# Kernel tuning notes

Hardware: AMD Instinct MI355X
Metric: run time of the kernel (lower is better)

## Reference

```python
import jax, jax.numpy as jnp
import numpy as np

B, T_PAST, T_FUT, GH, GW = 256, 20, 30, 100, 100
HID = 32  # past_encoder_dim


def gru_cell(x, h, w_ih, w_hh, b_ih, b_hh):
    # torch nn.GRU single-cell math; weights [3H, in], [3H, H]
    gi = x @ w_ih.T + b_ih
    gh = h @ w_hh.T + b_hh
    i_r, i_z, i_n = jnp.split(gi, 3, axis=-1)
    h_r, h_z, h_n = jnp.split(gh, 3, axis=-1)
    r = jax.nn.sigmoid(i_r + h_r)
    zg = jax.nn.sigmoid(i_z + h_z)
    n = jnp.tanh(i_n + r * h_n)
    return (1.0 - zg) * n + zg * h


def bilinear(grid, q):
    # grid [B,H,W,C]; q [B,2], dim 0 -> height, dim 1 -> width (matches torch code)
    Bn, Hh, Ww, C = grid.shape
    fy = jnp.clip(jnp.floor(q[:, 0]), 0.0, Hh - 2).astype(jnp.int32)
    fx = jnp.clip(jnp.floor(q[:, 1]), 0.0, Ww - 2).astype(jnp.int32)
    ay = jnp.clip(q[:, 0] - fy, 0.0, 1.0)[:, None]
    ax = jnp.clip(q[:, 1] - fx, 0.0, 1.0)[:, None]
    b = jnp.arange(Bn)
    tl = grid[b, fy, fx]
    tr = grid[b, fy, fx + 1]
    bl = grid[b, fy + 1, fx]
    br = grid[b, fy + 1, fx + 1]
    top = tl + ax * (tr - tl)
    bot = bl + ax * (br - bl)
    return top + ay * (bot - top)  # [B,C]


def setup_inputs() -> dict:
    key = jax.random.key(0)
    ks = jax.random.split(key, 24)
    s = 0.05
    f32 = jnp.float32
    inp = {
        'z': jax.random.normal(ks[0], (B, T_FUT, 2), f32),
        'player_past': jax.random.uniform(ks[1], (B, T_PAST, 2), f32) * (GH - 10),
        'lidar': jax.random.normal(ks[2], (B, GH, GW, 2), f32),
        'conv0_w': jax.random.normal(ks[3], (2, 2, 2, 32), f32) * s,   # HWIO
        'conv0_b': jnp.zeros((32,), f32),
        'conv1_w': jax.random.normal(ks[4], (2, 2, 32, 32), f32) * s,
        'conv1_b': jnp.zeros((32,), f32),
        'conv2_w': jax.random.normal(ks[5], (2, 2, 32, 32), f32) * s,
        'conv2_b': jnp.zeros((32,), f32),
        'conv3_w': jax.random.normal(ks[6], (2, 2, 32, 32), f32) * s,
        'conv3_b': jnp.zeros((32,), f32),
        'enc_wih': jax.random.normal(ks[7], (3 * HID, 2), f32) * s,
        'enc_whh': jax.random.normal(ks[8], (3 * HID, HID), f32) * s,
        'enc_bih': jnp.zeros((3 * HID,), f32),
        'enc_bhh': jnp.zeros((3 * HID,), f32),
        'dec_wih': jax.random.normal(ks[9], (3 * HID, HID + 2), f32) * s,
        'dec_whh': jax.random.normal(ks[10], (3 * HID, HID), f32) * s,
        'dec_bih': jnp.zeros((3 * HID,), f32),
        'dec_bhh': jnp.zeros((3 * HID,), f32),
        'mlp_w1': jax.random.normal(ks[11], (512, HID), f32) * s,
        'mlp_b1': jnp.zeros((512,), f32),
        'mlp_w2': jax.random.normal(ks[12], (4, 512), f32) * s,
        'mlp_b2': jnp.zeros((4,), f32),
    }
    return inp


def reference(z, player_past, lidar,
              conv0_w, conv0_b, conv1_w, conv1_b, conv2_w, conv2_b, conv3_w, conv3_b,
              enc_wih, enc_whh, enc_bih, enc_bhh,
              dec_wih, dec_whh, dec_bih, dec_bhh,
              mlp_w1, mlp_b1, mlp_w2, mlp_b2):
    # field model: ZeroPad2d((0,1,0,1)) + Conv 2x2 + ReLU, x4 -> same-size NHWC conv
    v = lidar
    for w, b in ((conv0_w, conv0_b), (conv1_w, conv1_b), (conv2_w, conv2_b), (conv3_w, conv3_b)):
        v = jax.nn.relu(jax.lax.conv_general_dilated(
            v, w, (1, 1), [(0, 1), (0, 1)],
            dimension_numbers=('NHWC', 'HWIO', 'NHWC')) + b)
    context_lidar = v  # [B,GH,GW,32]

    # past encoder GRU; last output of single-layer GRU == final hidden
    h0 = jnp.zeros((z.shape[0], HID), z.dtype)
    def enc_step(h, x_t):
        return gru_cell(x_t, h, enc_wih, enc_whh, enc_bih, enc_bhh), None
    h_enc, _ = jax.lax.scan(enc_step, h0, jnp.swapaxes(player_past, 0, 1))

    y_tm2 = player_past[:, -2, :]
    y_tm1 = player_past[:, -1, :]

    def dec_step(carry, z_t):
        h, y1, y2 = carry
        interp_t = bilinear(context_lidar, y1)                 # [B,32]
        x = jnp.concatenate([y1, interp_t], axis=-1)            # [B,34]
        h = gru_cell(x, h, dec_wih, dec_whh, dec_bih, dec_bhh)
        # locscale_mlp: Linear(32,512) -> Linear(512,4) (no ReLU between, per source)
        ls = (h @ mlp_w1.T + mlp_b1) @ mlp_w2.T + mlp_b2
        loc = ls[:, :2]
        scale = jax.nn.softplus(ls[:, 2:])
        y_t = 2.0 * y1 - y2 + loc + scale * z_t                 # verlet + affine sample
        return (h, y_t, y1), (y_t, scale)

    _, (ys, scales) = jax.lax.scan(dec_step, (h_enc, y_tm1, y_tm2), jnp.swapaxes(z, 0, 1))
    y = jnp.swapaxes(ys, 0, 1)          # [B,T,2]
    scales = jnp.swapaxes(scales, 0, 1)  # [B,T,2]
    logabsdet = jnp.sum(jnp.log(jnp.abs(jnp.prod(scales, axis=-2))), axis=-1)  # [B]
    return (y, logabsdet)
```

## Files before the change

### kernel.cpp

```cpp
#include <hip/hip_runtime.h>
#include <math.h>

typedef __attribute__((ext_vector_type(8))) short    short8;
typedef __attribute__((ext_vector_type(4))) float    f32x4;
typedef __attribute__((ext_vector_type(4))) unsigned uint4v;

#define FRAG0 256

__device__ __forceinline__ unsigned short f2bf(float f) {
    unsigned u = __builtin_bit_cast(unsigned, f);
    u = u + 0x7fffu + ((u >> 16) & 1u);
    return (unsigned short)(u >> 16);
}
__device__ __forceinline__ unsigned packRNE(float hi, float lo) {
    return (unsigned)f2bf(lo) | ((unsigned)f2bf(hi) << 16);
}
__device__ __forceinline__ unsigned pack_trunc(float hi, float lo) {
    return __builtin_amdgcn_perm(__builtin_bit_cast(unsigned, hi),
                                 __builtin_bit_cast(unsigned, lo), 0x07060302u);
}
__device__ __forceinline__ float rfl(float x) {
    return __builtin_bit_cast(float, __builtin_amdgcn_readfirstlane(__builtin_bit_cast(int, x)));
}
__device__ __forceinline__ f32x4 mfma16(short8 a, short8 b, f32x4 c) {
    return __builtin_amdgcn_mfma_f32_16x16x32_bf16(a, b, c, 0, 0, 0);
}
__device__ __forceinline__ unsigned bperm(int addr, unsigned v) {
    return (unsigned)__builtin_amdgcn_ds_bpermute(addr, (int)v);
}
template<int PAT>
__device__ __forceinline__ float swzXf(float v) {
    return __builtin_bit_cast(float, __builtin_amdgcn_ds_swizzle(__builtin_bit_cast(int, v), PAT));
}
__device__ __forceinline__ unsigned swz1u(unsigned v){ return (unsigned)__builtin_amdgcn_ds_swizzle((int)v, 0x041F); }
__device__ __forceinline__ float sigf(float x) { return __builtin_amdgcn_rcpf(1.f + __expf(-x)); }
__device__ __forceinline__ float tanhfast(float x) {
    float e = __expf(2.f * x);
    return 1.f - 2.f * __builtin_amdgcn_rcpf(e + 1.f);
}
__device__ __forceinline__ f32x4 ld4(const float* p) { return *(const f32x4*)p; }

__device__ __forceinline__ void packC(unsigned* P, f32x4 a0, f32x4 a1, bool oob) {
    float r0 = fmaxf(a0[0], 0.f), r1 = fmaxf(a0[1], 0.f), r2 = fmaxf(a0[2], 0.f), r3 = fmaxf(a0[3], 0.f);
    float s0 = fmaxf(a1[0], 0.f), s1 = fmaxf(a1[1], 0.f), s2 = fmaxf(a1[2], 0.f), s3 = fmaxf(a1[3], 0.f);
    P[0] = pack_trunc(r1, r0); P[1] = pack_trunc(r3, r2);
    P[2] = pack_trunc(s1, s0); P[3] = pack_trunc(s3, s2);
    if (oob) { P[0] = 0u; P[1] = 0u; P[2] = 0u; P[3] = 0u; }
}

__global__ __launch_bounds__(256) void r2p2_prep(
    const float* __restrict__ w0, const float* __restrict__ w1,
    const float* __restrict__ w2, const float* __restrict__ w3,
    const float* __restrict__ enc_whh,
    const float* __restrict__ dec_wih, const float* __restrict__ dec_whh,
    const float* __restrict__ mw1, const float* __restrict__ mb1,
    const float* __restrict__ mw2, const float* __restrict__ mb2,
    float* __restrict__ wsf, unsigned* __restrict__ wsu) {
    const int tid = threadIdx.x, bx = blockIdx.x;
    if (bx == 0) {
        __shared__ float red[64];
        if (tid < 128) {
            int k = tid & 31, j = tid >> 5;
            const float* w2r = mw2 + j * 512;
            float a0 = 0.f, a1 = 0.f, a2 = 0.f, a3 = 0.f;
#pragma unroll 4
            for (int m = 0; m < 512; m += 4) {
                a0 = fmaf(w2r[m],     mw1[m * 32 + k],       a0);
                a1 = fmaf(w2r[m + 1], mw1[(m + 1) * 32 + k], a1);
                a2 = fmaf(w2r[m + 2], mw1[(m + 2) * 32 + k], a2);
                a3 = fmaf(w2r[m + 3], mw1[(m + 3) * 32 + k], a3);
            }
            wsf[j * 32 + k] = (a0 + a1) + (a2 + a3);
        } else if (tid < 192) {
            int t = tid - 128;
            int j = t & 3, ch = t >> 2;
            const float* w2c = mw2 + j * 512 + ch * 32;
            const float* b1c = mb1 + ch * 32;
            float p = 0.f;
#pragma unroll 8
            for (int m = 0; m < 32; ++m) p = fmaf(w2c[m], b1c[m], p);
            red[t] = p;
        }
        __syncthreads();
        if (tid < 4) {
            float c = mb2[tid];
#pragma unroll
            for (int i = 0; i < 16; ++i) c += red[tid + i * 4];
            wsf[128 + tid] = c;
        }
        return;
    }
    int base = (bx - 1) * 416;
    for (int c = base + tid; c < base + 416 && c < 2816; c += 256) {
        int f = c >> 6, lane = c & 63;
        int n = lane & 15, q = lane >> 4;
        int pc0 = ((n >> 2) << 3) | (n & 3);
        float v[8];
        if (f < 2) {
            int co = pc0 + f * 4;
#pragma unroll
            for (int j = 0; j < 8; ++j) v[j] = (q == 0) ? w0[j * 32 + co] : 0.f;
        } else if (f < 26) {
            int t = f - 2;
            const float* W = (t < 8) ? w1 : (t < 16) ? w2 : w3;
            t &= 7;
            int mt = t >> 2, ks = t & 3, co = pc0 + mt * 4;
#pragma unroll
            for (int j = 0; j < 8; ++j) v[j] = W[(ks * 32 + q * 8 + j) * 32 + co];
        } else if (f < 32) {
            int t = f - 26, gate = t >> 1, mt = t & 1;
            int row = gate * 32 + pc0 + mt * 4;
#pragma unroll
            for (int j = 0; j < 8; ++j) v[j] = dec_wih[row * 34 + 2 + q * 8 + j];
        } else if (f < 38) {
            int t = f - 32, gate = t >> 1, mt = t & 1;
            int row = gate * 32 + pc0 + mt * 4;
#pragma unroll
            for (int j = 0; j < 8; ++j) v[j] = dec_whh[row * 32 + q * 8 + j];
        } else {
            int t = f - 38, gate = t >> 1, mt = t & 1;
            int row = gate * 32 + pc0 + mt * 4;
#pragma unroll
            for (int j = 0; j < 8; ++j) v[j] = enc_whh[row * 32 + q * 8 + j];
        }
        uint4v u;
        u[0] = packRNE(v[1], v[0]); u[1] = packRNE(v[3], v[2]);
        u[2] = packRNE(v[5], v[4]); u[3] = packRNE(v[7], v[6]);
        *(uint4v*)(wsu + FRAG0 + f * 256 + lane * 4) = u;
    }
}

__global__ __launch_bounds__(256)
void r2p2_main(
    const float* __restrict__ z, const float* __restrict__ past, const float* __restrict__ lidar,
    const float* __restrict__ b0, const float* __restrict__ b1,
    const float* __restrict__ b2, const float* __restrict__ b3,
    const float* __restrict__ enc_wih, const float* __restrict__ enc_bih, const float* __restrict__ enc_bhh,
    const float* __restrict__ dec_wih, const float* __restrict__ dec_bih, const float* __restrict__ dec_bhh,
    const float* __restrict__ wsf, const unsigned* __restrict__ wsu,
    float* __restrict__ out) {

    const int tid = threadIdx.x, b = blockIdx.x;
    const int wid = tid >> 6, lane = tid & 63;
    const int n = lane & 15, q = lane >> 4, e = n & 1;

    __shared__ __align__(16) unsigned sLID[104 * 104];
    __shared__ __align__(16) float PASTs[40];
    __shared__ __align__(16) float ZVs[64];

    if (wid != 0) {
        int st = tid - 64;
        if (st < 60) ZVs[st] = z[b * 60 + st];
        for (int i = st; i < 816; i += 192) {
            int idx = (i < 416) ? (10400 + i) : ((((i - 416) >> 2) * 104) + 100 + ((i - 416) & 3));
            sLID[idx] = 0u;
        }
        const float4* lp4 = (const float4*)(lidar + (size_t)b * 20000);
#pragma unroll 4
        for (int i = st; i < 5000; i += 192) {
            int r = (int)(((unsigned)i * 5243u) >> 18);
            int c2 = i - r * 50;
            float4 v = lp4[i];
            int o = r * 104 + 2 * c2;
            sLID[o]     = pack_trunc(v.y, v.x);
            sLID[o + 1] = pack_trunc(v.w, v.z);
        }
        __syncthreads();
        return;
    }

    uint4v FR[44];
#pragma unroll
    for (int f = 0; f < 44; ++f) FR[f] = *(const uint4v*)(wsu + FRAG0 + f * 256 + lane * 4);
#define FRG(f) __builtin_bit_cast(short8, FR[f])

    f32x4 cb0[2], cb1[2], cb2[2], cb3[2], gbR[2], gbZ[2], gbNi[2], gbNh[2];
    f32x4 egR[2], egZ[2], egNh[2];
#pragma unroll
    for (int mt = 0; mt < 2; ++mt) {
        int o = q * 8 + mt * 4;
        cb0[mt] = ld4(b0 + o); cb1[mt] = ld4(b1 + o); cb2[mt] = ld4(b2 + o); cb3[mt] = ld4(b3 + o);
        gbR[mt]  = ld4(dec_bih + o)      + ld4(dec_bhh + o);
        gbZ[mt]  = ld4(dec_bih + 32 + o) + ld4(dec_bhh + 32 + o);
        gbNi[mt] = ld4(dec_bih + 64 + o);
        gbNh[mt] = ld4(dec_bhh + 64 + o);
        egR[mt]  = ld4(enc_bih + o)      + ld4(enc_bhh + o);
        egZ[mt]  = ld4(enc_bih + 32 + o) + ld4(enc_bhh + 32 + o);
        egNh[mt] = ld4(enc_bhh + 64 + o);
    }
    f32x4 ebni = ld4(enc_bih + 64 + q * 8 + e * 4);
    float2 wxr[4], wxz[4], wxn[4], wexr[4], wexz[4], wexn[4];
#pragma unroll
    for (int r = 0; r < 4; ++r) {
        int c = q * 8 + e * 4 + r;
        wxr[r]  = *(const float2*)(dec_wih + c * 34);
        wxz[r]  = *(const float2*)(dec_wih + (32 + c) * 34);
        wxn[r]  = *(const float2*)(dec_wih + (64 + c) * 34);
        wexr[r] = *(const float2*)(enc_wih + c * 2);
        wexz[r] = *(const float2*)(enc_wih + (32 + c) * 2);
        wexn[r] = *(const float2*)(enc_wih + (64 + c) * 2);
    }
    short8 Am = (short8)0;
    if (n < 4) {
#pragma unroll
        for (int j = 0; j < 8; ++j) Am[j] = (short)f2bf(wsf[n * 32 + q * 8 + j]);
    }
    f32x4 mcv = {0.f, 0.f, 0.f, 0.f};
    if (q == 0) mcv = *(const f32x4*)(wsf + 128);

    if (lane < 20) *(float2*)&PASTs[2 * lane] = *(const float2*)(past + b * 40 + 2 * lane);
    float q0 = past[b * 40 + 38], q1 = past[b * 40 + 39];
    float p0 = past[b * 40 + 36], p1 = past[b * 40 + 37];
    asm volatile("s_waitcnt lgkmcnt(0)" ::: "memory");

    float hq[4] = {0.f, 0.f, 0.f, 0.f};
    short8 hfr = (short8)0;
#pragma unroll 1
    for (int t = 0; t < 20; ++t) {
        float2 xp = *(const float2*)&PASTs[2 * t];
        f32x4 gr0 = mfma16(FRG(38), hfr, egR[0]),  gr1 = mfma16(FRG(39), hfr, egR[1]);
        f32x4 gz0 = mfma16(FRG(40), hfr, egZ[0]),  gz1 = mfma16(FRG(41), hfr, egZ[1]);
        f32x4 gh0 = mfma16(FRG(42), hfr, egNh[0]), gh1 = mfma16(FRG(43), hfr, egNh[1]);
        f32x4 grS = e ? gr1 : gr0, gzS = e ? gz1 : gz0, ghS = e ? gh1 : gh0;
        float hn[4];
#pragma unroll
        for (int r = 0; r < 4; ++r) {
            float rp = grS[r] + xp.x * wexr[r].x + xp.y * wexr[r].y;
            float zp = gzS[r] + xp.x * wexz[r].x + xp.y * wexz[r].y;
            float pi = ebni[r] + xp.x * wexn[r].x + xp.y * wexn[r].y;
            float rr = sigf(rp), zz = sigf(zp);
            float tn = tanhfast(fmaf(rr, ghS[r], pi));
            float hv = tn + zz * (hq[r] - tn);
            hq[r] = hv; hn[r] = hv;
        }
        unsigned hu0 = packRNE(hn[1], hn[0]), hu1 = packRNE(hn[3], hn[2]);
        unsigned po0 = swz1u(hu0), po1 = swz1u(hu1);
        uint4v hv4;
        hv4[0] = e ? po0 : hu0; hv4[1] = e ? po1 : hu1;
        hv4[2] = e ? hu0 : po0; hv4[3] = e ? hu1 : po1;
        hfr = __builtin_bit_cast(short8, hv4);
    }

    __syncthreads();

    int py0a = n / 5, px0a = n % 5;
    int pe0b = (16 + n < 25) ? 16 + n : 24;
    int py0b = pe0b / 5, px0b = pe0b - py0b * 5;
    int ofs0a[4], ofs0b[4];
#pragma unroll
    for (int tp = 0; tp < 4; ++tp) {
        ofs0a[tp] = (py0a + (tp >> 1)) * 104 + px0a + (tp & 1);
        ofs0b[tp] = (py0b + (tp >> 1)) * 104 + px0b + (tp & 1);
    }
    int py1 = n >> 2, px1 = n & 3;
    int adr1[4], sel1m[4];
#pragma unroll
    for (int ks = 0; ks < 4; ++ks) {
        int p = (py1 + (ks >> 1)) * 5 + px1 + (ks & 1);
        adr1[ks] = (q * 16 + (p & 15)) * 4;
        sel1m[ks] = (p >= 16);
    }
    int pe2 = (n < 9) ? n : 8, py2 = pe2 / 3, px2 = pe2 - py2 * 3;
    int adr2[4];
#pragma unroll
    for (int ks = 0; ks < 4; ++ks) adr2[ks] = (q * 16 + (py2 + (ks >> 1)) * 4 + px2 + (ks & 1)) * 4;
    int pe3 = n & 3, py3 = pe3 >> 1, px3 = pe3 & 1;
    int adr3[4];
#pragma unroll
    for (int ks = 0; ks < 4; ++ks) adr3[ks] = (q * 16 + (py3 + (ks >> 1)) * 3 + px3 + (ks & 1)) * 4;
    const f32x4 zf4 = {0.f, 0.f, 0.f, 0.f};
    float la = 0.f;

#pragma unroll 1
    for (int t = 0; t < 30; ++t) {
        float2 zv = *(const float2*)&ZVs[2 * t];
        float f0 = fminf(fmaxf(floorf(q0), 0.f), 98.f);
        float f1v = fminf(fmaxf(floorf(q1), 0.f), 98.f);
        int fy = (int)f0, fx = (int)f1v;
        float ay = fminf(fmaxf(q0 - f0, 0.f), 1.f);
        float ax = fminf(fmaxf(q1 - f1v, 0.f), 1.f);
        int base = fy * 104 + fx;
        int limy = 100 - fy, limx = 100 - fx;

        short8 bfa = (short8)0, bfb = (short8)0;
        if (q == 0) {
            uint4v ua, ub;
#pragma unroll
            for (int tp = 0; tp < 4; ++tp) { ua[tp] = sLID[base + ofs0a[tp]]; ub[tp] = sLID[base + ofs0b[tp]]; }
            bfa = __builtin_bit_cast(short8, ua);
            bfb = __builtin_bit_cast(short8, ub);
        }
        f32x4 ca0 = mfma16(FRG(0), bfa, cb0[0]);
        f32x4 ca1 = mfma16(FRG(1), bfa, cb0[1]);
        f32x4 cB0 = mfma16(FRG(0), bfb, cb0[0]);
        f32x4 cB1 = mfma16(FRG(1), bfb, cb0[1]);
        unsigned Pa[4], Pb[4];
        packC(Pa, ca0, ca1, (py0a >= limy) || (px0a >= limx));
        packC(Pb, cB0, cB1, (py0b >= limy) || (px0b >= limx));

        short8 bf1[4];
#pragma unroll
        for (int ks = 0; ks < 4; ++ks) {
            uint4v bu;
#pragma unroll
            for (int u = 0; u < 4; ++u) {
                unsigned va = bperm(adr1[ks], Pa[u]);
                unsigned vb = bperm(adr1[ks], Pb[u]);
                bu[u] = sel1m[ks] ? vb : va;
            }
            bf1[ks] = __builtin_bit_cast(short8, bu);
        }
        {
            f32x4 aA = mfma16(FRG(2), bf1[0], cb1[0]); aA = mfma16(FRG(3), bf1[1], aA);
            f32x4 aB = mfma16(FRG(4), bf1[2], zf4);    aB = mfma16(FRG(5), bf1[3], aB);
            f32x4 bA = mfma16(FRG(6), bf1[0], cb1[1]); bA = mfma16(FRG(7), bf1[1], bA);
            f32x4 bB = mfma16(FRG(8), bf1[2], zf4);    bB = mfma16(FRG(9), bf1[3], bB);
            f32x4 o0 = aA + aB, o1 = bA + bB;
            packC(Pa, o0, o1, (py1 >= limy) || (px1 >= limx));
        }

        short8 bf2v[4];
#pragma unroll
        for (int ks = 0; ks < 4; ++ks) {
            uint4v bu;
#pragma unroll
            for (int u = 0; u < 4; ++u) bu[u] = bperm(adr2[ks], Pa[u]);
            bf2v[ks] = __builtin_bit_cast(short8, bu);
        }
        {
            f32x4 aA = mfma16(FRG(10), bf2v[0], cb2[0]); aA = mfma16(FRG(11), bf2v[1], aA);
            f32x4 aB = mfma16(FRG(12), bf2v[2], zf4);    aB = mfma16(FRG(13), bf2v[3], aB);
            f32x4 bA = mfma16(FRG(14), bf2v[0], cb2[1]); bA = mfma16(FRG(15), bf2v[1], bA);
            f32x4 bB = mfma16(FRG(16), bf2v[2], zf4);    bB = mfma16(FRG(17), bf2v[3], bB);
            f32x4 o0 = aA + aB, o1 = bA + bB;
            packC(Pb, o0, o1, (py2 >= limy) || (px2 >= limx));
        }

        short8 bf3v[4];
#pragma unroll
        for (int ks = 0; ks < 4; ++ks) {
            uint4v bu;
#pragma unroll
            for (int u = 0; u < 4; ++u) bu[u] = bperm(adr3[ks], Pb[u]);
            bf3v[ks] = __builtin_bit_cast(short8, bu);
        }
        short8 xf;
        {
            f32x4 aA = mfma16(FRG(18), bf3v[0], cb3[0]); aA = mfma16(FRG(19), bf3v[1], aA);
            f32x4 aB = mfma16(FRG(20), bf3v[2], zf4);    aB = mfma16(FRG(21), bf3v[3], aB);
            f32x4 bA = mfma16(FRG(22), bf3v[0], cb3[1]); bA = mfma16(FRG(23), bf3v[1], bA);
            f32x4 bB = mfma16(FRG(24), bf3v[2], zf4);    bB = mfma16(FRG(25), bf3v[3], bB);
            f32x4 o0 = aA + aB, o1 = bA + bB;
            float wy = (n & 2) ? ay : 1.f - ay;
            float wx = (n & 1) ? ax : 1.f - ax;
            float w = wy * wx;
            float t0[4], t1[4];
#pragma unroll
            for (int r = 0; r < 4; ++r) { t0[r] = fmaxf(o0[r], 0.f) * w; t1[r] = fmaxf(o1[r], 0.f) * w; }
#pragma unroll
            for (int r = 0; r < 4; ++r) {
                float a1 = swzXf<0x041F>(t0[r]), a2 = swzXf<0x081F>(t0[r]), a3 = swzXf<0x0C1F>(t0[r]);
                t0[r] = (t0[r] + a1) + (a2 + a3);
                float b1v = swzXf<0x041F>(t1[r]), b2v = swzXf<0x081F>(t1[r]), b3v = swzXf<0x0C1F>(t1[r]);
                t1[r] = (t1[r] + b1v) + (b2v + b3v);
            }
            uint4v xu;
            xu[0] = packRNE(t0[1], t0[0]); xu[1] = packRNE(t0[3], t0[2]);
            xu[2] = packRNE(t1[1], t1[0]); xu[3] = packRNE(t1[3], t1[2]);
            xf = __builtin_bit_cast(short8, xu);
        }

        f32x4 gr0 = mfma16(FRG(26), xf, gbR[0]); gr0 = mfma16(FRG(32), hfr, gr0);
        f32x4 gr1 = mfma16(FRG(27), xf, gbR[1]); gr1 = mfma16(FRG(33), hfr, gr1);
        f32x4 gz0 = mfma16(FRG(28), xf, gbZ[0]); gz0 = mfma16(FRG(34), hfr, gz0);
        f32x4 gz1 = mfma16(FRG(29), xf, gbZ[1]); gz1 = mfma16(FRG(35), hfr, gz1);
        f32x4 gi0 = mfma16(FRG(30), xf, gbNi[0]);
        f32x4 gi1 = mfma16(FRG(31), xf, gbNi[1]);
        f32x4 gh0 = mfma16(FRG(36), hfr, gbNh[0]);
        f32x4 gh1 = mfma16(FRG(37), hfr, gbNh[1]);
        f32x4 grS = e ? gr1 : gr0, gzS = e ? gz1 : gz0, giS = e ? gi1 : gi0, ghS = e ? gh1 : gh0;
        float hn[4];
#pragma unroll
        for (int r = 0; r < 4; ++r) {
            float rp = grS[r] + q0 * wxr[r].x + q1 * wxr[r].y;
            float zp = gzS[r] + q0 * wxz[r].x + q1 * wxz[r].y;
            float pi = giS[r] + q0 * wxn[r].x + q1 * wxn[r].y;
            float rr = sigf(rp), zz = sigf(zp);
            float tn = tanhfast(fmaf(rr, ghS[r], pi));
            float hv = tn + zz * (hq[r] - tn);
            hq[r] = hv; hn[r] = hv;
        }
        unsigned hu0 = packRNE(hn[1], hn[0]), hu1 = packRNE(hn[3], hn[2]);
        unsigned po0 = swz1u(hu0), po1 = swz1u(hu1);
        uint4v hv4;
        hv4[0] = e ? po0 : hu0; hv4[1] = e ? po1 : hu1;
        hv4[2] = e ? hu0 : po0; hv4[3] = e ? hu1 : po1;
        hfr = __builtin_bit_cast(short8, hv4);

        f32x4 ls = mfma16(Am, hfr, mcv);
        float l2 = ls[2], l3 = ls[3];
        float s0 = fmaxf(l2, 0.f) + __logf(1.f + __expf(-fabsf(l2)));
        float s1 = fmaxf(l3, 0.f) + __logf(1.f + __expf(-fabsf(l3)));
        float ny0 = 2.f * q0 - p0 + ls[0] + s0 * zv.x;
        float ny1 = 2.f * q1 - p1 + ls[1] + s1 * zv.y;
        if (lane == 0) {
            float2 o2 = {ny0, ny1};
            *(float2*)(out + b * 60 + 2 * t) = o2;
        }
        la += __logf(s0 * s1);
        p0 = q0; p1 = q1;
        q0 = rfl(ny0); q1 = rfl(ny1);
    }
    if (lane == 0) out[15360 + b] = la;
#undef FRG
}

extern "C" void kernel_launch(void* const* d_in, const int* in_sizes, int n_in,
                              void* d_out, int out_size, void* d_ws, size_t ws_size,
                              hipStream_t stream) {
    const float* z    = (const float*)d_in[0];
    const float* past = (const float*)d_in[1];
    const float* lid  = (const float*)d_in[2];
    const float* c0w = (const float*)d_in[3];  const float* c0b = (const float*)d_in[4];
    const float* c1w = (const float*)d_in[5];  const float* c1b = (const float*)d_in[6];
    const float* c2w = (const float*)d_in[7];  const float* c2b = (const float*)d_in[8];
    const float* c3w = (const float*)d_in[9];  const float* c3b = (const float*)d_in[10];
    const float* ewih = (const float*)d_in[11]; const float* ewhh = (const float*)d_in[12];
    const float* ebih = (const float*)d_in[13]; const float* ebhh = (const float*)d_in[14];
    const float* dwih = (const float*)d_in[15]; const float* dwhh = (const float*)d_in[16];
    const float* dbih = (const float*)d_in[17]; const float* dbhh = (const float*)d_in[18];
    const float* mw1 = (const float*)d_in[19]; const float* mb1 = (const float*)d_in[20];
    const float* mw2 = (const float*)d_in[21]; const float* mb2 = (const float*)d_in[22];
    float* out = (float*)d_out;
    float* wsf = (float*)d_ws;
    unsigned* wsu = (unsigned*)d_ws;

    r2p2_prep<<<8, 256, 0, stream>>>(c0w, c1w, c2w, c3w, ewhh, dwih, dwhh,
                                     mw1, mb1, mw2, mb2, wsf, wsu);
    r2p2_main<<<256, 256, 0, stream>>>(z, past, lid, c0b, c1b, c2b, c3b,
                                       ewih, ebih, ebhh, dwih, dbih, dbhh,
                                       wsf, wsu, out);
}
```

Before: 184.1 us.

## Restructure conv pyramid with DPP shuffles and hoist hidden-state GRU matmuls

The conv stack is reorganised so that layer 0 is computed on a 4x4 receptive layout directly from nine shared-memory loads per patch, which removes the bpermute gather between layers 0 and 1. Layer 2's gather becomes DPP row shifts (shl 1/4/5). The ds_swizzle reductions and exchanges become DPP xor moves. The hidden-state GRU matmuls for the next step are issued right after h updates, so they overlap with the softplus and position update and come off the critical path of the next iteration. The cost is more layer-0 MFMAs (4 patches instead of 2) and higher register pressure from the carried accumulators. The DPP row-shift lane mapping has to match the new patch layout exactly.

Result: faster. 179.5 us (-2.5%).

```diff
diff --git a/kernel.cpp b/kernel.cpp
--- a/kernel.cpp
+++ b/kernel.cpp
@@ -28,11 +28,21 @@
 __device__ __forceinline__ unsigned bperm(int addr, unsigned v) {
     return (unsigned)__builtin_amdgcn_ds_bpermute(addr, (int)v);
 }
-template<int PAT>
-__device__ __forceinline__ float swzXf(float v) {
-    return __builtin_bit_cast(float, __builtin_amdgcn_ds_swizzle(__builtin_bit_cast(int, v), PAT));
-}
-__device__ __forceinline__ unsigned swz1u(unsigned v){ return (unsigned)__builtin_amdgcn_ds_swizzle((int)v, 0x041F); }
+template<int CTRL>
+__device__ __forceinline__ unsigned dppu(unsigned v) {
+    return (unsigned)__builtin_amdgcn_update_dpp((int)v, (int)v, CTRL, 0xF, 0xF, false);
+}
+template<int CTRL>
+__device__ __forceinline__ float dppf(float v) {
+    int i = __builtin_bit_cast(int, v);
+    return __builtin_bit_cast(float, __builtin_amdgcn_update_dpp(i, i, CTRL, 0xF, 0xF, false));
+}
+#define DPP_XOR1 0xB1
+#define DPP_XOR2 0x4E
+#define DPP_SHL1 0x101
+#define DPP_SHL4 0x104
+#define DPP_SHL5 0x105
+
 __device__ __forceinline__ float sigf(float x) { return __builtin_amdgcn_rcpf(1.f + __expf(-x)); }
 __device__ __forceinline__ float tanhfast(float x) {
     float e = __expf(2.f * x);
@@ -234,40 +244,29 @@
             hq[r] = hv; hn[r] = hv;
         }
         unsigned hu0 = packRNE(hn[1], hn[0]), hu1 = packRNE(hn[3], hn[2]);
-        unsigned po0 = swz1u(hu0), po1 = swz1u(hu1);
+        unsigned po0 = dppu<DPP_XOR1>(hu0), po1 = dppu<DPP_XOR1>(hu1);
         uint4v hv4;
         hv4[0] = e ? po0 : hu0; hv4[1] = e ? po1 : hu1;
         hv4[2] = e ? hu0 : po0; hv4[3] = e ? hu1 : po1;
         hfr = __builtin_bit_cast(short8, hv4);
     }
 
+    f32x4 hr0 = mfma16(FRG(32), hfr, gbR[0]);
+    f32x4 hr1 = mfma16(FRG(33), hfr, gbR[1]);
+    f32x4 hz0 = mfma16(FRG(34), hfr, gbZ[0]);
+    f32x4 hz1 = mfma16(FRG(35), hfr, gbZ[1]);
+    f32x4 hgn0 = mfma16(FRG(36), hfr, gbNh[0]);
+    f32x4 hgn1 = mfma16(FRG(37), hfr, gbNh[1]);
+
     __syncthreads();
 
-    int py0a = n / 5, px0a = n % 5;
-    int pe0b = (16 + n < 25) ? 16 + n : 24;
-    int py0b = pe0b / 5, px0b = pe0b - py0b * 5;
-    int ofs0a[4], ofs0b[4];
-#pragma unroll
-    for (int tp = 0; tp < 4; ++tp) {
-        ofs0a[tp] = (py0a + (tp >> 1)) * 104 + px0a + (tp & 1);
-        ofs0b[tp] = (py0b + (tp >> 1)) * 104 + px0b + (tp & 1);
-    }
-    int py1 = n >> 2, px1 = n & 3;
-    int adr1[4], sel1m[4];
-#pragma unroll
-    for (int ks = 0; ks < 4; ++ks) {
-        int p = (py1 + (ks >> 1)) * 5 + px1 + (ks & 1);
-        adr1[ks] = (q * 16 + (p & 15)) * 4;
-        sel1m[ks] = (p >= 16);
-    }
-    int pe2 = (n < 9) ? n : 8, py2 = pe2 / 3, px2 = pe2 - py2 * 3;
-    int adr2[4];
-#pragma unroll
-    for (int ks = 0; ks < 4; ++ks) adr2[ks] = (q * 16 + (py2 + (ks >> 1)) * 4 + px2 + (ks & 1)) * 4;
-    int pe3 = n & 3, py3 = pe3 >> 1, px3 = pe3 & 1;
+    const int py1 = n >> 2, px1 = n & 3;
+    const int woff = py1 * 104 + px1;
+    const int py3 = (n >> 1) & 1, px3 = n & 1;
     int adr3[4];
 #pragma unroll
-    for (int ks = 0; ks < 4; ++ks) adr3[ks] = (q * 16 + (py3 + (ks >> 1)) * 3 + px3 + (ks & 1)) * 4;
+    for (int ks = 0; ks < 4; ++ks)
+        adr3[ks] = (q * 16 + (py3 + (ks >> 1)) * 4 + px3 + (ks & 1)) * 4;
     const f32x4 zf4 = {0.f, 0.f, 0.f, 0.f};
     float la = 0.f;
 
@@ -282,34 +281,35 @@
         int base = fy * 104 + fx;
         int limy = 100 - fy, limx = 100 - fx;
 
-        short8 bfa = (short8)0, bfb = (short8)0;
+        unsigned W9[9];
         if (q == 0) {
-            uint4v ua, ub;
-#pragma unroll
-            for (int tp = 0; tp < 4; ++tp) { ua[tp] = sLID[base + ofs0a[tp]]; ub[tp] = sLID[base + ofs0b[tp]]; }
-            bfa = __builtin_bit_cast(short8, ua);
-            bfb = __builtin_bit_cast(short8, ub);
-        }
-        f32x4 ca0 = mfma16(FRG(0), bfa, cb0[0]);
-        f32x4 ca1 = mfma16(FRG(1), bfa, cb0[1]);
-        f32x4 cB0 = mfma16(FRG(0), bfb, cb0[0]);
-        f32x4 cB1 = mfma16(FRG(1), bfb, cb0[1]);
-        unsigned Pa[4], Pb[4];
-        packC(Pa, ca0, ca1, (py0a >= limy) || (px0a >= limx));
-        packC(Pb, cB0, cB1, (py0b >= limy) || (px0b >= limx));
-
+            int bw = base + woff;
+#pragma unroll
+            for (int ry = 0; ry < 3; ++ry)
+#pragma unroll
+                for (int rx = 0; rx < 3; ++rx)
+                    W9[ry * 3 + rx] = sLID[bw + ry * 104 + rx];
+        }
         short8 bf1[4];
 #pragma unroll
         for (int ks = 0; ks < 4; ++ks) {
-            uint4v bu;
-#pragma unroll
-            for (int u = 0; u < 4; ++u) {
-                unsigned va = bperm(adr1[ks], Pa[u]);
-                unsigned vb = bperm(adr1[ks], Pb[u]);
-                bu[u] = sel1m[ks] ? vb : va;
+            int dy = ks >> 1, dx = ks & 1;
+            uint4v u = (uint4v)0u;
+            if (q == 0) {
+                int wb = dy * 3 + dx;
+                u[0] = W9[wb];     u[1] = W9[wb + 1];
+                u[2] = W9[wb + 3]; u[3] = W9[wb + 4];
             }
-            bf1[ks] = __builtin_bit_cast(short8, bu);
-        }
+            short8 bq = __builtin_bit_cast(short8, u);
+            f32x4 c0 = mfma16(FRG(0), bq, cb0[0]);
+            f32x4 c1 = mfma16(FRG(1), bq, cb0[1]);
+            unsigned P[4];
+            packC(P, c0, c1, (py1 + dy >= limy) || (px1 + dx >= limx));
+            uint4v up; up[0] = P[0]; up[1] = P[1]; up[2] = P[2]; up[3] = P[3];
+            bf1[ks] = __builtin_bit_cast(short8, up);
+        }
+
+        unsigned Pa[4];
         {
             f32x4 aA = mfma16(FRG(2), bf1[0], cb1[0]); aA = mfma16(FRG(3), bf1[1], aA);
             f32x4 aB = mfma16(FRG(4), bf1[2], zf4);    aB = mfma16(FRG(5), bf1[3], aB);
@@ -320,20 +320,28 @@
         }
 
         short8 bf2v[4];
-#pragma unroll
-        for (int ks = 0; ks < 4; ++ks) {
-            uint4v bu;
-#pragma unroll
-            for (int u = 0; u < 4; ++u) bu[u] = bperm(adr2[ks], Pa[u]);
-            bf2v[ks] = __builtin_bit_cast(short8, bu);
-        }
+        {
+            uint4v g0, g1, g2, g3;
+#pragma unroll
+            for (int u = 0; u < 4; ++u) {
+                g0[u] = Pa[u];
+                g1[u] = dppu<DPP_SHL1>(Pa[u]);
+                g2[u] = dppu<DPP_SHL4>(Pa[u]);
+                g3[u] = dppu<DPP_SHL5>(Pa[u]);
+            }
+            bf2v[0] = __builtin_bit_cast(short8, g0);
+            bf2v[1] = __builtin_bit_cast(short8, g1);
+            bf2v[2] = __builtin_bit_cast(short8, g2);
+            bf2v[3] = __builtin_bit_cast(short8, g3);
+        }
+        unsigned Pb[4];
         {
             f32x4 aA = mfma16(FRG(10), bf2v[0], cb2[0]); aA = mfma16(FRG(11), bf2v[1], aA);
             f32x4 aB = mfma16(FRG(12), bf2v[2], zf4);    aB = mfma16(FRG(13), bf2v[3], aB);
             f32x4 bA = mfma16(FRG(14), bf2v[0], cb2[1]); bA = mfma16(FRG(15), bf2v[1], bA);
             f32x4 bB = mfma16(FRG(16), bf2v[2], zf4);    bB = mfma16(FRG(17), bf2v[3], bB);
             f32x4 o0 = aA + aB, o1 = bA + bB;
-            packC(Pb, o0, o1, (py2 >= limy) || (px2 >= limx));
+            packC(Pb, o0, o1, (py1 >= limy) || (px1 >= limx));
         }
 
         short8 bf3v[4];
@@ -359,10 +367,8 @@
             for (int r = 0; r < 4; ++r) { t0[r] = fmaxf(o0[r], 0.f) * w; t1[r] = fmaxf(o1[r], 0.f) * w; }
 #pragma unroll
             for (int r = 0; r < 4; ++r) {
-                float a1 = swzXf<0x041F>(t0[r]), a2 = swzXf<0x081F>(t0[r]), a3 = swzXf<0x0C1F>(t0[r]);
-                t0[r] = (t0[r] + a1) + (a2 + a3);
-                float b1v = swzXf<0x041F>(t1[r]), b2v = swzXf<0x081F>(t1[r]), b3v = swzXf<0x0C1F>(t1[r]);
-                t1[r] = (t1[r] + b1v) + (b2v + b3v);
+                t0[r] += dppf<DPP_XOR1>(t0[r]); t1[r] += dppf<DPP_XOR1>(t1[r]);
+                t0[r] += dppf<DPP_XOR2>(t0[r]); t1[r] += dppf<DPP_XOR2>(t1[r]);
             }
             uint4v xu;
             xu[0] = packRNE(t0[1], t0[0]); xu[1] = packRNE(t0[3], t0[2]);
@@ -370,15 +376,13 @@
             xf = __builtin_bit_cast(short8, xu);
         }
 
-        f32x4 gr0 = mfma16(FRG(26), xf, gbR[0]); gr0 = mfma16(FRG(32), hfr, gr0);
-        f32x4 gr1 = mfma16(FRG(27), xf, gbR[1]); gr1 = mfma16(FRG(33), hfr, gr1);
-        f32x4 gz0 = mfma16(FRG(28), xf, gbZ[0]); gz0 = mfma16(FRG(34), hfr, gz0);
-        f32x4 gz1 = mfma16(FRG(29), xf, gbZ[1]); gz1 = mfma16(FRG(35), hfr, gz1);
+        f32x4 gr0 = mfma16(FRG(26), xf, hr0);
+        f32x4 gr1 = mfma16(FRG(27), xf, hr1);
+        f32x4 gz0 = mfma16(FRG(28), xf, hz0);
+        f32x4 gz1 = mfma16(FRG(29), xf, hz1);
         f32x4 gi0 = mfma16(FRG(30), xf, gbNi[0]);
         f32x4 gi1 = mfma16(FRG(31), xf, gbNi[1]);
-        f32x4 gh0 = mfma16(FRG(36), hfr, gbNh[0]);
-        f32x4 gh1 = mfma16(FRG(37), hfr, gbNh[1]);
-        f32x4 grS = e ? gr1 : gr0, gzS = e ? gz1 : gz0, giS = e ? gi1 : gi0, ghS = e ? gh1 : gh0;
+        f32x4 grS = e ? gr1 : gr0, gzS = e ? gz1 : gz0, giS = e ? gi1 : gi0, ghS = e ? hgn1 : hgn0;
         float hn[4];
 #pragma unroll
         for (int r = 0; r < 4; ++r) {
@@ -391,13 +395,21 @@
             hq[r] = hv; hn[r] = hv;
         }
         unsigned hu0 = packRNE(hn[1], hn[0]), hu1 = packRNE(hn[3], hn[2]);
-        unsigned po0 = swz1u(hu0), po1 = swz1u(hu1);
+        unsigned po0 = dppu<DPP_XOR1>(hu0), po1 = dppu<DPP_XOR1>(hu1);
         uint4v hv4;
         hv4[0] = e ? po0 : hu0; hv4[1] = e ? po1 : hu1;
         hv4[2] = e ? hu0 : po0; hv4[3] = e ? hu1 : po1;
         hfr = __builtin_bit_cast(short8, hv4);
 
         f32x4 ls = mfma16(Am, hfr, mcv);
+
+        hr0 = mfma16(FRG(32), hfr, gbR[0]);
+        hr1 = mfma16(FRG(33), hfr, gbR[1]);
+        hz0 = mfma16(FRG(34), hfr, gbZ[0]);
+        hz1 = mfma16(FRG(35), hfr, gbZ[1]);
+        hgn0 = mfma16(FRG(36), hfr, gbNh[0]);
+        hgn1 = mfma16(FRG(37), hfr, gbNh[1]);
+
         float l2 = ls[2], l3 = ls[3];
         float s0 = fmaxf(l2, 0.f) + __logf(1.f + __expf(-fabsf(l2)));
         float s1 = fmaxf(l3, 0.f) + __logf(1.f + __expf(-fabsf(l3)));
```
